# Performance work log

Measured on AMD Instinct MI355X. Metric: run time of the kernel, lower is better.

Reference implementation:

```python
import jax, jax.numpy as jnp
import numpy as np

N = 50000   # num_nodes
D = 256     # embedding_dim
R = 3       # num relations / views
E = 800000  # random edges per relation (before self-loops)
T = 8192    # target node indices
LN_EPS = 1e-5


def _build_relation(key):
    """Random graph + gcn_norm with self-loops (symmetric D^-1/2 A D^-1/2)."""
    k1, k2, k3 = jax.random.split(key, 3)
    src = jax.random.randint(k1, (E,), 0, N)
    dst = jax.random.randint(k2, (E,), 0, N)
    w = jax.random.uniform(k3, (E,))
    loop = jnp.arange(N)
    row = jnp.concatenate([src, loop])
    col = jnp.concatenate([dst, loop])
    val = jnp.concatenate([w, jnp.ones(N, jnp.float32)])
    deg = jax.ops.segment_sum(val, col, num_segments=N)
    dinv = jnp.where(deg > 0, jax.lax.rsqrt(deg), 0.0)
    val = dinv[row] * val * dinv[col]
    return row.astype(jnp.int32), col.astype(jnp.int32), val.astype(jnp.float32)


def setup_inputs() -> dict:
    key = jax.random.key(0)
    ks = jax.random.split(key, 12)
    rows, cols, vals = [], [], []
    for i in range(R):
        r, c, v = _build_relation(jax.random.fold_in(ks[0], i))
        rows.append(r); cols.append(c); vals.append(v)
    s = 1.0 / np.sqrt(D)
    inp = dict(
        node_emb=jax.random.normal(ks[1], (N, D), jnp.float32),
        W_pre=jax.random.normal(ks[2], (D, D), jnp.float32) * s,
        b_pre=jnp.zeros((D,), jnp.float32),
        g_pre=jnp.ones((D,), jnp.float32),
        be_pre=jnp.zeros((D,), jnp.float32),
        W_view=jax.random.normal(ks[3], (R, D, D), jnp.float32) * s,
        b_view=jnp.zeros((R, D), jnp.float32),
        g_view=jnp.ones((R, D), jnp.float32),
        be_view=jnp.zeros((R, D), jnp.float32),
        att_w=jax.random.normal(ks[4], (D, 1), jnp.float32) * s,
        att_b=jnp.zeros((1,), jnp.float32),
        g_fin=jnp.ones((D,), jnp.float32),
        be_fin=jnp.zeros((D,), jnp.float32),
        vals=jnp.stack(vals),            # [R, E+N]
        rows=jnp.stack(rows),            # [R, E+N] int32
        cols=jnp.stack(cols),            # [R, E+N] int32
        target_idx=jax.random.randint(ks[5], (T,), 0, N).astype(jnp.int32),
        hops=2,
    )
    return inp


def _ln(x, g, b):
    mu = jnp.mean(x, axis=-1, keepdims=True)
    var = jnp.mean(jnp.square(x - mu), axis=-1, keepdims=True)
    return (x - mu) * jax.lax.rsqrt(var + LN_EPS) * g + b


def _spmm(row, col, val, x):
    # out[i] = sum_{e: row[e]=i} val[e] * x[col[e]]
    return jax.ops.segment_sum(val[:, None] * x[col], row, num_segments=x.shape[0])


def reference(node_emb, W_pre, b_pre, g_pre, be_pre, W_view, b_view, g_view,
              be_view, att_w, att_b, g_fin, be_fin, vals, rows, cols,
              target_idx, hops):
    n = node_emb.shape[0]
    # pre_encoder: Linear + LayerNorm + GELU (exact erf gelu like torch default)
    x_graph = jax.nn.gelu(_ln(node_emb @ W_pre + b_pre, g_pre, be_pre), approximate=False)
    embeddings = []
    for i in range(rows.shape[0]):
        out = x_graph
        for _ in range(hops):
            out = _spmm(rows[i], cols[i], vals[i], out)
        out = jax.nn.gelu(_ln(out @ W_view[i] + b_view[i], g_view[i], be_view[i]),
                          approximate=False)
        embeddings.append(out)
    stack = jnp.stack(embeddings, axis=1)              # [N, R, D]
    scores = stack @ att_w + att_b                     # [N, R, 1]
    alpha = jax.nn.softmax(scores, axis=1)
    fused = jnp.sum(alpha * stack, axis=1)             # [N, D]
    control = x_graph[n - 1][None, :]
    final = jnp.concatenate([fused[: n - 1], control], axis=0)
    final = _ln(final, g_fin, be_fin)
    return final[target_idx]
```

## Files before the change

kernel.cpp:

```cpp
#include <hip/hip_runtime.h>
#include <hip/hip_bf16.h>
#include <math.h>

#define DD 256
#define BUCKET_SHIFT 9
#define BROWS 512
#define CHUNK_A 4096
#define CBLK_SHIFT 13

typedef __attribute__((ext_vector_type(8))) short short8;
typedef __attribute__((ext_vector_type(4))) float f32x4;

__device__ __forceinline__ float gelu_exact(float x) {
    return 0.5f * x * (1.0f + erff(x * 0.70710678118654752f));
}
__device__ __forceinline__ float b2f(unsigned short u) {
    unsigned int v = ((unsigned int)u) << 16;
    return __builtin_bit_cast(float, v);
}
__device__ __forceinline__ unsigned short f2b(float f) {
    __hip_bfloat16 h = __float2bfloat16(f);
    return __builtin_bit_cast(unsigned short, h);
}

__global__ __launch_bounds__(256) void part_hist(const int* __restrict__ rows,
                                                 int* __restrict__ bh,
                                                 int nnz, int NB, int nblkA) {
    int rel = blockIdx.y, blk = blockIdx.x;
    __shared__ int h[128];
    for (int b = threadIdx.x; b < NB; b += 256) h[b] = 0;
    __syncthreads();
    int base = blk * CHUNK_A;
    #pragma unroll
    for (int k = 0; k < CHUNK_A / 256; ++k) {
        int i = base + k * 256 + threadIdx.x;
        if (i < nnz) atomicAdd(&h[rows[(size_t)rel * nnz + i] >> BUCKET_SHIFT], 1);
    }
    __syncthreads();
    for (int b = threadIdx.x; b < NB; b += 256)
        bh[((size_t)(rel * NB + b)) * nblkA + blk] = h[b];
}

__global__ __launch_bounds__(256) void scan1(const int* __restrict__ cnt,
                                             int* __restrict__ rp, int* __restrict__ psum,
                                             int N, int nchunks) {
    int rel = blockIdx.x / nchunks;
    int chunk = blockIdx.x % nchunks;
    const int* c = cnt + (size_t)rel * N;
    int* out = rp + (size_t)rel * (N + 1);
    int tid = threadIdx.x, lane = tid & 63, wv = tid >> 6;
    __shared__ int wsum[4];
    int base = chunk * 1024 + tid * 4;
    int v[4];
    if (base + 3 < N) {
        int4 t4 = *(const int4*)(c + base);
        v[0] = t4.x; v[1] = t4.y; v[2] = t4.z; v[3] = t4.w;
    } else {
        #pragma unroll
        for (int q = 0; q < 4; ++q) v[q] = (base + q < N) ? c[base + q] : 0;
    }
    int tsum = v[0] + v[1] + v[2] + v[3];
    int x = tsum;
    #pragma unroll
    for (int off = 1; off < 64; off <<= 1) {
        int t = __shfl_up(x, off, 64);
        if (lane >= off) x += t;
    }
    if (lane == 63) wsum[wv] = x;
    __syncthreads();
    int woff = 0;
    #pragma unroll
    for (int k = 0; k < 4; ++k) if (k < wv) woff += wsum[k];
    int run = woff + x - tsum;
    #pragma unroll
    for (int q = 0; q < 4; ++q) {
        if (base + q < N) out[base + q] = run;
        run += v[q];
    }
    if (tid == 255) psum[rel * nchunks + chunk] = woff + x;
}

__global__ __launch_bounds__(256) void scan2(int* __restrict__ psum, int* __restrict__ rp,
                                             int N, int nchunks, int R) {
    int rel = threadIdx.x >> 6, lane = threadIdx.x & 63;
    if (rel >= R) return;
    int v = (lane < nchunks) ? psum[rel * nchunks + lane] : 0;
    int x = v;
    #pragma unroll
    for (int off = 1; off < 64; off <<= 1) {
        int t = __shfl_up(x, off, 64);
        if (lane >= off) x += t;
    }
    if (lane < nchunks) psum[rel * nchunks + lane] = x - v;
    if (lane == 63) rp[(size_t)rel * (N + 1) + N] = x;
}

__global__ __launch_bounds__(256) void scan3(int* __restrict__ rp, const int* __restrict__ psum,
                                             int N, int nchunks) {
    int rel = blockIdx.y;
    int i = blockIdx.x * 256 + threadIdx.x;
    if (i >= N) return;
    rp[(size_t)rel * (N + 1) + i] += psum[rel * nchunks + (i >> 10)];
}

__global__ __launch_bounds__(256) void part_scatter(
    const int* __restrict__ rows, const int* __restrict__ cols,
    const float* __restrict__ vals, const int* __restrict__ bhs,
    int2* __restrict__ staged, int nnz, int NB, int nblkA) {
    int rel = blockIdx.y, blk = blockIdx.x;
    __shared__ int cur[128];
    for (int b = threadIdx.x; b < NB; b += 256)
        cur[b] = bhs[((size_t)(rel * NB + b)) * nblkA + blk];
    __syncthreads();
    int base = blk * CHUNK_A;
    #pragma unroll
    for (int k = 0; k < CHUNK_A / 256; ++k) {
        int i = base + k * 256 + threadIdx.x;
        if (i < nnz) {
            int r = rows[(size_t)rel * nnz + i];
            unsigned c = (unsigned)cols[(size_t)rel * nnz + i];
            float v = vals[(size_t)rel * nnz + i];
            int pos = atomicAdd(&cur[r >> BUCKET_SHIFT], 1);
            int2 pr;
            pr.x = (int)(((unsigned)r << 16) | c);
            pr.y = __float_as_int(v);
            staged[pos] = pr;
        }
    }
}

__global__ __launch_bounds__(512) void bucket_build(
    const int2* __restrict__ staged, const int* __restrict__ bhs,
    int* __restrict__ rp, int2* __restrict__ spair,
    int nnz, int N, int NB, int nblkA, int R) {
    int rel = blockIdx.y, b = blockIdx.x;
    int start = bhs[((size_t)(rel * NB + b)) * nblkA];
    int nb1 = rel * NB + b + 1;
    int end = (nb1 < R * NB) ? bhs[(size_t)nb1 * nblkA] : R * nnz;
    int csr_base = start - rel * nnz;
    int rowbase = b << BUCKET_SHIFT;
    __shared__ int cnt2[BROWS * 8];
    __shared__ int wsum[8];
    int t = threadIdx.x, lane = t & 63, wv = t >> 6;
    #pragma unroll
    for (int q = 0; q < 8; ++q) cnt2[t + q * BROWS] = 0;
    __syncthreads();
    for (int i = start + t; i < end; i += 512) {
        unsigned p = (unsigned)staged[i].x;
        int rb = (int)(p >> 16) - rowbase;
        int cb = (int)(p & 0xFFFFu) >> CBLK_SHIFT;
        atomicAdd(&cnt2[rb * 8 + cb], 1);
    }
    __syncthreads();
    int c[8];
    int v = 0;
    #pragma unroll
    for (int q = 0; q < 8; ++q) { c[q] = cnt2[t * 8 + q]; v += c[q]; }
    int x = v;
    #pragma unroll
    for (int off = 1; off < 64; off <<= 1) {
        int tt = __shfl_up(x, off, 64);
        if (lane >= off) x += tt;
    }
    if (lane == 63) wsum[wv] = x;
    __syncthreads();
    int woff = 0;
    #pragma unroll
    for (int k = 0; k < 8; ++k) if (k < wv) woff += wsum[k];
    int excl = woff + x - v;
    __syncthreads();
    int run = excl;
    #pragma unroll
    for (int q = 0; q < 8; ++q) { cnt2[t * 8 + q] = run; run += c[q]; }
    int gr = rowbase + t;
    if (gr <= N) rp[(size_t)rel * (N + 1) + gr] = csr_base + excl;
    __syncthreads();
    for (int i = start + t; i < end; i += 512) {
        int2 s = staged[i];
        unsigned p = (unsigned)s.x;
        int rb = (int)(p >> 16) - rowbase;
        int col = (int)(p & 0xFFFFu);
        int pos = atomicAdd(&cnt2[rb * 8 + (col >> CBLK_SHIFT)], 1);
        int2 pr;
        pr.x = col;
        pr.y = s.y;
        spair[(size_t)rel * nnz + csr_base + pos] = pr;
    }
}

__global__ __launch_bounds__(256) void transpose_cast_w(
    const float* __restrict__ Wp, const float* __restrict__ Wv,
    unsigned short* __restrict__ wt) {
    __shared__ float tile[32][33];
    int m = blockIdx.y;
    int tb = blockIdx.x;
    int k0 = (tb & 7) * 32, n0 = (tb >> 3) * 32;
    const float* W = (m == 0) ? Wp : (Wv + (size_t)(m - 1) * 65536);
    int tx = threadIdx.x & 31, ty = threadIdx.x >> 5;
    #pragma unroll
    for (int i = 0; i < 4; ++i)
        tile[ty + 8 * i][tx] = W[(size_t)(k0 + ty + 8 * i) * 256 + n0 + tx];
    __syncthreads();
    #pragma unroll
    for (int i = 0; i < 4; ++i)
        wt[(size_t)m * 65536 + (size_t)(n0 + ty + 8 * i) * 256 + k0 + tx] =
            f2b(tile[tx][ty + 8 * i]);
}

template <bool A_BF16, bool OUT_BF16>
__global__ __launch_bounds__(512) void gemm_wlds(
    const void* __restrict__ Aptr, const unsigned short* __restrict__ Wt,
    const float* __restrict__ bias, const float* __restrict__ gamma,
    const float* __restrict__ beta, void* __restrict__ outp, int M, int ntiles,
    size_t aStrideB, size_t wStride, int pStride, size_t oStrideB)
{
    __shared__ __align__(16) unsigned short Wl[256 * 256];
    __shared__ float Pb[DD], Pg[DD], Pe[DD];
    const int rel = blockIdx.y;
    const char* Abase = (const char*)Aptr + (size_t)rel * aStrideB;
    char* Obase = (char*)outp + (size_t)rel * oStrideB;
    const unsigned short* Wtr = Wt + (size_t)rel * wStride;
    const int tid = threadIdx.x;
    const int lane = tid & 63;
    const int wv = tid >> 6;
    if (tid < DD) {
        Pb[tid] = bias[rel * pStride + tid];
        Pg[tid] = gamma[rel * pStride + tid];
        Pe[tid] = beta[rel * pStride + tid];
    }
    {
        int n = tid >> 1;
        int half = tid & 1;
        const unsigned short* src = Wtr + (size_t)n * DD + half * 128;
        #pragma unroll
        for (int c = 0; c < 16; ++c) {
            int c16 = half * 16 + c;
            short8 v = *(const short8*)(src + c * 8);
            *(short8*)(Wl + n * DD + ((c16 ^ (n & 7)) << 3)) = v;
        }
    }
    __syncthreads();

    const int cl = lane & 15, g = lane >> 4;

    for (int tile = blockIdx.x; tile < ntiles; tile += gridDim.x) {
        const int rbase = tile * 128 + wv * 16;
        const int arow = rbase + cl;
        const bool rok = arow < M;
        f32x4 acc[16];
        #pragma unroll
        for (int j = 0; j < 16; ++j) acc[j] = (f32x4){0.f, 0.f, 0.f, 0.f};

        #pragma unroll 2
        for (int ks = 0; ks < 8; ++ks) {
            short8 af = (short8){0,0,0,0,0,0,0,0};
            if (rok) {
                if (A_BF16) {
                    af = *(const short8*)((const unsigned short*)Abase +
                            (size_t)arow * DD + ks * 32 + g * 8);
                } else {
                    const float* ap = (const float*)Abase + (size_t)arow * DD + ks * 32 + g * 8;
                    float4 f0 = *(const float4*)ap;
                    float4 f1 = *(const float4*)(ap + 4);
                    af = (short8){(short)f2b(f0.x), (short)f2b(f0.y), (short)f2b(f0.z), (short)f2b(f0.w),
                                  (short)f2b(f1.x), (short)f2b(f1.y), (short)f2b(f1.z), (short)f2b(f1.w)};
                }
            }
            int c16 = 4 * ks + g;
            #pragma unroll
            for (int j = 0; j < 16; ++j) {
                int n = j * 16 + cl;
                short8 bf = *(const short8*)(Wl + n * DD + ((c16 ^ (n & 7)) << 3));
                acc[j] = __builtin_amdgcn_mfma_f32_16x16x32_bf16(af, bf, acc[j], 0, 0, 0);
            }
        }

        #pragma unroll
        for (int q = 0; q < 4; ++q) {
            float yv[16];
            float s = 0.f, ss = 0.f;
            #pragma unroll
            for (int j = 0; j < 16; ++j) {
                float y = acc[j][q] + Pb[cl + 16 * j];
                yv[j] = y; s += y; ss += y * y;
            }
            #pragma unroll
            for (int off = 1; off < 16; off <<= 1) {
                s  += __shfl_xor(s,  off, 16);
                ss += __shfl_xor(ss, off, 16);
            }
            float mean = s * (1.0f / DD);
            float var  = ss * (1.0f / DD) - mean * mean;
            float rstd = rsqrtf(var + 1e-5f);
            int row = rbase + g * 4 + q;
            if (row < M) {
                #pragma unroll
                for (int j = 0; j < 16; ++j) {
                    int col = cl + 16 * j;
                    float o = gelu_exact((yv[j] - mean) * rstd * Pg[col] + Pe[col]);
                    if (OUT_BF16)
                        ((unsigned short*)Obase)[(size_t)row * DD + col] = f2b(o);
                    else
                        ((float*)Obase)[(size_t)row * DD + col] = o;
                }
            }
        }
    }
}

__global__ __launch_bounds__(256) void spmm_bf(
    const int* __restrict__ rp, const int2* __restrict__ spair,
    const unsigned short* __restrict__ x, unsigned short* __restrict__ y, int N)
{
    int r = blockIdx.x * 4 + (threadIdx.x >> 6);
    if (r >= N) return;
    int lane = threadIdx.x & 63;
    int half = lane >> 5;
    int hl = lane & 31;
    int s = rp[r], e = rp[r + 1];
    float acc[8];
    #pragma unroll
    for (int k = 0; k < 8; ++k) acc[k] = 0.f;
    int j = s;
    for (; j + 4 <= e; j += 4) {
        int2 pA = spair[j + half];
        int2 pB = spair[j + 2 + half];
        short8 xa = *(const short8*)(x + (size_t)pA.x * DD + hl * 8);
        short8 xb = *(const short8*)(x + (size_t)pB.x * DD + hl * 8);
        float va = __int_as_float(pA.y), vb = __int_as_float(pB.y);
        #pragma unroll
        for (int k = 0; k < 8; ++k) {
            acc[k] += va * b2f((unsigned short)xa[k]);
            acc[k] += vb * b2f((unsigned short)xb[k]);
        }
    }
    for (; j + 2 <= e; j += 2) {
        int2 p = spair[j + half];
        short8 xv = *(const short8*)(x + (size_t)p.x * DD + hl * 8);
        float v = __int_as_float(p.y);
        #pragma unroll
        for (int k = 0; k < 8; ++k) acc[k] += v * b2f((unsigned short)xv[k]);
    }
    if (j < e && half == 0) {
        int2 p = spair[j];
        short8 xv = *(const short8*)(x + (size_t)p.x * DD + hl * 8);
        float v = __int_as_float(p.y);
        #pragma unroll
        for (int k = 0; k < 8; ++k) acc[k] += v * b2f((unsigned short)xv[k]);
    }
    #pragma unroll
    for (int k = 0; k < 8; ++k) acc[k] += __shfl_xor(acc[k], 32, 64);
    if (half == 0) {
        short8 o;
        #pragma unroll
        for (int k = 0; k < 8; ++k) o[k] = (short)f2b(acc[k]);
        *(short8*)(y + (size_t)r * DD + hl * 8) = o;
    }
}

__global__ __launch_bounds__(256) void spmm_tgt_bf(
    const int* __restrict__ rp0, const int2* __restrict__ spair0,
    const unsigned short* __restrict__ x0, const int* __restrict__ tgt,
    unsigned short* __restrict__ y0, int T, int N, int nnz)
{
    int rel = blockIdx.y;
    const int* rp = rp0 + (size_t)rel * (N + 1);
    const int2* spair = spair0 + (size_t)rel * nnz;
    const unsigned short* x = x0 + (size_t)rel * N * DD;
    unsigned short* y = y0 + (size_t)rel * T * DD;
    int sI = blockIdx.x * 4 + (threadIdx.x >> 6);
    if (sI >= T) return;
    int lane = threadIdx.x & 63;
    int half = lane >> 5;
    int hl = lane & 31;
    int r = tgt[sI];
    int s = rp[r], e = rp[r + 1];
    float acc[8];
    #pragma unroll
    for (int k = 0; k < 8; ++k) acc[k] = 0.f;
    int j = s;
    for (; j + 4 <= e; j += 4) {
        int2 pA = spair[j + half];
        int2 pB = spair[j + 2 + half];
        short8 xa = *(const short8*)(x + (size_t)pA.x * DD + hl * 8);
        short8 xb = *(const short8*)(x + (size_t)pB.x * DD + hl * 8);
        float va = __int_as_float(pA.y), vb = __int_as_float(pB.y);
        #pragma unroll
        for (int k = 0; k < 8; ++k) {
            acc[k] += va * b2f((unsigned short)xa[k]);
            acc[k] += vb * b2f((unsigned short)xb[k]);
        }
    }
    for (; j + 2 <= e; j += 2) {
        int2 p = spair[j + half];
        short8 xv = *(const short8*)(x + (size_t)p.x * DD + hl * 8);
        float v = __int_as_float(p.y);
        #pragma unroll
        for (int k = 0; k < 8; ++k) acc[k] += v * b2f((unsigned short)xv[k]);
    }
    if (j < e && half == 0) {
        int2 p = spair[j];
        short8 xv = *(const short8*)(x + (size_t)p.x * DD + hl * 8);
        float v = __int_as_float(p.y);
        #pragma unroll
        for (int k = 0; k < 8; ++k) acc[k] += v * b2f((unsigned short)xv[k]);
    }
    #pragma unroll
    for (int k = 0; k < 8; ++k) acc[k] += __shfl_xor(acc[k], 32, 64);
    if (half == 0) {
        short8 o;
        #pragma unroll
        for (int k = 0; k < 8; ++k) o[k] = (short)f2b(acc[k]);
        *(short8*)(y + (size_t)sI * DD + hl * 8) = o;
    }
}

__global__ __launch_bounds__(256) void final_kernel(
    const unsigned short* __restrict__ emb, size_t emb_stride,
    const unsigned short* __restrict__ xg,
    const float* __restrict__ att_w, const float* __restrict__ att_b,
    const float* __restrict__ g_fin, const float* __restrict__ be_fin,
    const int* __restrict__ tgt, float* __restrict__ out, int N, int T)
{
    int sI = blockIdx.x * 4 + (threadIdx.x >> 6);
    if (sI >= T) return;
    int lane = threadIdx.x & 63;
    int t = tgt[sI];
    float4 row;
    if (t == N - 1) {
        ushort4 xv = *(const ushort4*)(xg + (size_t)t * DD + lane * 4);
        row.x = b2f(xv.x); row.y = b2f(xv.y); row.z = b2f(xv.z); row.w = b2f(xv.w);
    } else {
        ushort4 u0 = *(const ushort4*)(emb + (size_t)sI * DD + lane * 4);
        ushort4 u1 = *(const ushort4*)(emb + emb_stride + (size_t)sI * DD + lane * 4);
        ushort4 u2 = *(const ushort4*)(emb + 2 * emb_stride + (size_t)sI * DD + lane * 4);
        float4 e0 = make_float4(b2f(u0.x), b2f(u0.y), b2f(u0.z), b2f(u0.w));
        float4 e1 = make_float4(b2f(u1.x), b2f(u1.y), b2f(u1.z), b2f(u1.w));
        float4 e2 = make_float4(b2f(u2.x), b2f(u2.y), b2f(u2.z), b2f(u2.w));
        float4 aw = *(const float4*)(att_w + lane * 4);
        float s0 = e0.x*aw.x + e0.y*aw.y + e0.z*aw.z + e0.w*aw.w;
        float s1 = e1.x*aw.x + e1.y*aw.y + e1.z*aw.z + e1.w*aw.w;
        float s2 = e2.x*aw.x + e2.y*aw.y + e2.z*aw.z + e2.w*aw.w;
        #pragma unroll
        for (int off = 32; off > 0; off >>= 1) {
            s0 += __shfl_xor(s0, off, 64);
            s1 += __shfl_xor(s1, off, 64);
            s2 += __shfl_xor(s2, off, 64);
        }
        float ab = att_b[0];
        s0 += ab; s1 += ab; s2 += ab;
        float m = fmaxf(s0, fmaxf(s1, s2));
        float w0 = expf(s0 - m), w1 = expf(s1 - m), w2 = expf(s2 - m);
        float inv = 1.0f / (w0 + w1 + w2);
        w0 *= inv; w1 *= inv; w2 *= inv;
        row.x = w0*e0.x + w1*e1.x + w2*e2.x;
        row.y = w0*e0.y + w1*e1.y + w2*e2.y;
        row.z = w0*e0.z + w1*e1.z + w2*e2.z;
        row.w = w0*e0.w + w1*e1.w + w2*e2.w;
    }
    float s  = row.x + row.y + row.z + row.w;
    float ss = row.x*row.x + row.y*row.y + row.z*row.z + row.w*row.w;
    #pragma unroll
    for (int off = 32; off > 0; off >>= 1) {
        s  += __shfl_xor(s,  off, 64);
        ss += __shfl_xor(ss, off, 64);
    }
    float mean = s * (1.0f / DD);
    float var  = ss * (1.0f / DD) - mean * mean;
    float rstd = rsqrtf(var + 1e-5f);
    float4 gg  = *(const float4*)(g_fin  + lane * 4);
    float4 be4 = *(const float4*)(be_fin + lane * 4);
    float4 o;
    o.x = (row.x - mean) * rstd * gg.x + be4.x;
    o.y = (row.y - mean) * rstd * gg.y + be4.y;
    o.z = (row.z - mean) * rstd * gg.z + be4.z;
    o.w = (row.w - mean) * rstd * gg.w + be4.w;
    *(float4*)(out + (size_t)sI * DD + lane * 4) = o;
}

extern "C" void kernel_launch(void* const* d_in, const int* in_sizes, int n_in,
                              void* d_out, int out_size, void* d_ws, size_t ws_size,
                              hipStream_t stream) {
    const float* node_emb = (const float*)d_in[0];
    const float* W_pre  = (const float*)d_in[1];
    const float* b_pre  = (const float*)d_in[2];
    const float* g_pre  = (const float*)d_in[3];
    const float* be_pre = (const float*)d_in[4];
    const float* W_view = (const float*)d_in[5];
    const float* b_view = (const float*)d_in[6];
    const float* g_view = (const float*)d_in[7];
    const float* be_view= (const float*)d_in[8];
    const float* att_w  = (const float*)d_in[9];
    const float* att_b  = (const float*)d_in[10];
    const float* g_fin  = (const float*)d_in[11];
    const float* be_fin = (const float*)d_in[12];
    const float* vals   = (const float*)d_in[13];
    const int*   rows   = (const int*)d_in[14];
    const int*   cols   = (const int*)d_in[15];
    const int*   tgt    = (const int*)d_in[16];

    const int N   = in_sizes[0] / DD;
    const int R   = in_sizes[5] / (DD * DD);
    const int nnz = in_sizes[13] / R;
    const int T   = in_sizes[16];

    const int NB    = (N + BROWS - 1) >> BUCKET_SHIFT;
    const int nblkA = (nnz + CHUNK_A - 1) / CHUNK_A;
    const int S     = R * NB * nblkA;
    const int nchS  = (S + 1023) / 1024;

    char* ws = (char*)d_ws;
    size_t off = 0;
    auto alloc = [&](size_t bytes) -> char* {
        char* p = ws + off;
        off += (bytes + 255) & ~(size_t)255;
        return p;
    };
    int*            rp     = (int*)alloc((size_t)R * (N + 1) * 4);
    int*            psum   = (int*)alloc(1024);
    int*            bhraw  = (int*)alloc((size_t)S * 4);
    int*            bhs    = (int*)alloc((size_t)(S + 1) * 4);
    int2*           spair  = (int2*)alloc((size_t)R * nnz * 8);
    unsigned short* xg_bf  = (unsigned short*)alloc((size_t)N * DD * 2);
    unsigned short* tmp_bf = (unsigned short*)alloc((size_t)R * N * DD * 2);
    unsigned short* ev_bf  = (unsigned short*)alloc((size_t)R * T * DD * 2);
    unsigned short* wt_bf  = (unsigned short*)alloc((size_t)(R + 1) * DD * DD * 2);
    int2* staged = (int2*)tmp_bf;
    (void)ws_size; (void)n_in; (void)out_size;

    part_hist<<<dim3(nblkA, R), 256, 0, stream>>>(rows, bhraw, nnz, NB, nblkA);
    scan1<<<nchS, 256, 0, stream>>>(bhraw, bhs, psum, S, nchS);
    scan2<<<1, 256, 0, stream>>>(psum, bhs, S, nchS, 1);
    scan3<<<dim3((S + 255) / 256, 1), 256, 0, stream>>>(bhs, psum, S, nchS);
    part_scatter<<<dim3(nblkA, R), 256, 0, stream>>>(rows, cols, vals, bhs, staged,
                                                     nnz, NB, nblkA);
    bucket_build<<<dim3(NB, R), 512, 0, stream>>>(staged, bhs, rp, spair,
                                                  nnz, N, NB, nblkA, R);

    transpose_cast_w<<<dim3(64, R + 1), 256, 0, stream>>>(W_pre, W_view, wt_bf);

    int ntiles_pre = (N + 127) / 128;
    int grid_pre = ntiles_pre < 256 ? ntiles_pre : 256;
    gemm_wlds<false, true><<<dim3(grid_pre, 1), 512, 0, stream>>>(
        node_emb, wt_bf, b_pre, g_pre, be_pre, xg_bf, N, ntiles_pre, 0, 0, 0, 0);

    for (int v = 0; v < R; ++v) {
        spmm_bf<<<(N + 3) / 4, 256, 0, stream>>>(rp + (size_t)v * (N + 1),
                                                 spair + (size_t)v * nnz, xg_bf,
                                                 tmp_bf + (size_t)v * N * DD, N);
    }

    spmm_tgt_bf<<<dim3((T + 3) / 4, R), 256, 0, stream>>>(rp, spair, tmp_bf, tgt,
                                                          ev_bf, T, N, nnz);

    int ntiles_v = (T + 127) / 128;
    gemm_wlds<true, true><<<dim3(ntiles_v, R), 512, 0, stream>>>(
        ev_bf, wt_bf + (size_t)DD * DD, b_view, g_view, be_view, ev_bf, T, ntiles_v,
        (size_t)T * DD * 2, (size_t)DD * DD, DD, (size_t)T * DD * 2);

    final_kernel<<<(T + 3) / 4, 256, 0, stream>>>(ev_bf, (size_t)T * DD, xg_bf,
                                                  att_w, att_b, g_fin, be_fin, tgt,
                                                  (float*)d_out, N, T);
}
```

Measured before the change: 340.1 us.

## Gather first-hop SpMM from FP8 copy of x_graph and shrink intermediate buffer

```diff
diff --git a/kernel.cpp b/kernel.cpp
--- a/kernel.cpp
+++ b/kernel.cpp
@@ -205,6 +205,21 @@
     for (int i = 0; i < 4; ++i)
         wt[(size_t)m * 65536 + (size_t)(n0 + ty + 8 * i) * 256 + k0 + tx] =
             f2b(tile[tx][ty + 8 * i]);
+}
+
+__global__ __launch_bounds__(256) void cast_f8(const unsigned short* __restrict__ xb,
+                                               unsigned char* __restrict__ xf, long n8) {
+    long i = (long)blockIdx.x * 256 + threadIdx.x;
+    if (i >= n8) return;
+    short8 v = *(const short8*)(xb + i * 8);
+    float f[8];
+    #pragma unroll
+    for (int k = 0; k < 8; ++k) f[k] = b2f((unsigned short)v[k]);
+    int d0 = __builtin_amdgcn_cvt_pk_fp8_f32(f[0], f[1], 0, false);
+    d0 = __builtin_amdgcn_cvt_pk_fp8_f32(f[2], f[3], d0, true);
+    int d1 = __builtin_amdgcn_cvt_pk_fp8_f32(f[4], f[5], 0, false);
+    d1 = __builtin_amdgcn_cvt_pk_fp8_f32(f[6], f[7], d1, true);
+    *(uint2*)(xf + i * 8) = make_uint2((unsigned)d0, (unsigned)d1);
 }
 
 template <bool A_BF16, bool OUT_BF16>
@@ -308,9 +323,9 @@
     }
 }
 
-__global__ __launch_bounds__(256) void spmm_bf(
+__global__ __launch_bounds__(256) void spmm_f8(
     const int* __restrict__ rp, const int2* __restrict__ spair,
-    const unsigned short* __restrict__ x, unsigned short* __restrict__ y, int N)
+    const unsigned char* __restrict__ x, unsigned short* __restrict__ y, int N)
 {
     int r = blockIdx.x * 4 + (threadIdx.x >> 6);
     if (r >= N) return;
@@ -325,28 +340,60 @@
     for (; j + 4 <= e; j += 4) {
         int2 pA = spair[j + half];
         int2 pB = spair[j + 2 + half];
-        short8 xa = *(const short8*)(x + (size_t)pA.x * DD + hl * 8);
-        short8 xb = *(const short8*)(x + (size_t)pB.x * DD + hl * 8);
+        uint2 ua = *(const uint2*)(x + (size_t)pA.x * DD + hl * 8);
+        uint2 ub = *(const uint2*)(x + (size_t)pB.x * DD + hl * 8);
         float va = __int_as_float(pA.y), vb = __int_as_float(pB.y);
-        #pragma unroll
-        for (int k = 0; k < 8; ++k) {
-            acc[k] += va * b2f((unsigned short)xa[k]);
-            acc[k] += vb * b2f((unsigned short)xb[k]);
-        }
+        float xa[8], xb[8];
+        xa[0] = __builtin_amdgcn_cvt_f32_fp8((int)ua.x, 0);
+        xa[1] = __builtin_amdgcn_cvt_f32_fp8((int)ua.x, 1);
+        xa[2] = __builtin_amdgcn_cvt_f32_fp8((int)ua.x, 2);
+        xa[3] = __builtin_amdgcn_cvt_f32_fp8((int)ua.x, 3);
+        xa[4] = __builtin_amdgcn_cvt_f32_fp8((int)ua.y, 0);
+        xa[5] = __builtin_amdgcn_cvt_f32_fp8((int)ua.y, 1);
+        xa[6] = __builtin_amdgcn_cvt_f32_fp8((int)ua.y, 2);
+        xa[7] = __builtin_amdgcn_cvt_f32_fp8((int)ua.y, 3);
+        xb[0] = __builtin_amdgcn_cvt_f32_fp8((int)ub.x, 0);
+        xb[1] = __builtin_amdgcn_cvt_f32_fp8((int)ub.x, 1);
+        xb[2] = __builtin_amdgcn_cvt_f32_fp8((int)ub.x, 2);
+        xb[3] = __builtin_amdgcn_cvt_f32_fp8((int)ub.x, 3);
+        xb[4] = __builtin_amdgcn_cvt_f32_fp8((int)ub.y, 0);
+        xb[5] = __builtin_amdgcn_cvt_f32_fp8((int)ub.y, 1);
+        xb[6] = __builtin_amdgcn_cvt_f32_fp8((int)ub.y, 2);
+        xb[7] = __builtin_amdgcn_cvt_f32_fp8((int)ub.y, 3);
+        #pragma unroll
+        for (int k = 0; k < 8; ++k) acc[k] += va * xa[k] + vb * xb[k];
     }
     for (; j + 2 <= e; j += 2) {
         int2 p = spair[j + half];
-        short8 xv = *(const short8*)(x + (size_t)p.x * DD + hl * 8);
+        uint2 ua = *(const uint2*)(x + (size_t)p.x * DD + hl * 8);
         float v = __int_as_float(p.y);
-        #pragma unroll
-        for (int k = 0; k < 8; ++k) acc[k] += v * b2f((unsigned short)xv[k]);
+        float xa[8];
+        xa[0] = __builtin_amdgcn_cvt_f32_fp8((int)ua.x, 0);
+        xa[1] = __builtin_amdgcn_cvt_f32_fp8((int)ua.x, 1);
+        xa[2] = __builtin_amdgcn_cvt_f32_fp8((int)ua.x, 2);
+        xa[3] = __builtin_amdgcn_cvt_f32_fp8((int)ua.x, 3);
+        xa[4] = __builtin_amdgcn_cvt_f32_fp8((int)ua.y, 0);
+        xa[5] = __builtin_amdgcn_cvt_f32_fp8((int)ua.y, 1);
+        xa[6] = __builtin_amdgcn_cvt_f32_fp8((int)ua.y, 2);
+        xa[7] = __builtin_amdgcn_cvt_f32_fp8((int)ua.y, 3);
+        #pragma unroll
+        for (int k = 0; k < 8; ++k) acc[k] += v * xa[k];
     }
     if (j < e && half == 0) {
         int2 p = spair[j];
-        short8 xv = *(const short8*)(x + (size_t)p.x * DD + hl * 8);
+        uint2 ua = *(const uint2*)(x + (size_t)p.x * DD + hl * 8);
         float v = __int_as_float(p.y);
-        #pragma unroll
-        for (int k = 0; k < 8; ++k) acc[k] += v * b2f((unsigned short)xv[k]);
+        float xa[8];
+        xa[0] = __builtin_amdgcn_cvt_f32_fp8((int)ua.x, 0);
+        xa[1] = __builtin_amdgcn_cvt_f32_fp8((int)ua.x, 1);
+        xa[2] = __builtin_amdgcn_cvt_f32_fp8((int)ua.x, 2);
+        xa[3] = __builtin_amdgcn_cvt_f32_fp8((int)ua.x, 3);
+        xa[4] = __builtin_amdgcn_cvt_f32_fp8((int)ua.y, 0);
+        xa[5] = __builtin_amdgcn_cvt_f32_fp8((int)ua.y, 1);
+        xa[6] = __builtin_amdgcn_cvt_f32_fp8((int)ua.y, 2);
+        xa[7] = __builtin_amdgcn_cvt_f32_fp8((int)ua.y, 3);
+        #pragma unroll
+        for (int k = 0; k < 8; ++k) acc[k] += v * xa[k];
     }
     #pragma unroll
     for (int k = 0; k < 8; ++k) acc[k] += __shfl_xor(acc[k], 32, 64);
@@ -359,15 +406,10 @@
 }
 
 __global__ __launch_bounds__(256) void spmm_tgt_bf(
-    const int* __restrict__ rp0, const int2* __restrict__ spair0,
-    const unsigned short* __restrict__ x0, const int* __restrict__ tgt,
-    unsigned short* __restrict__ y0, int T, int N, int nnz)
+    const int* __restrict__ rp, const int2* __restrict__ spair,
+    const unsigned short* __restrict__ x, const int* __restrict__ tgt,
+    unsigned short* __restrict__ y, int T)
 {
-    int rel = blockIdx.y;
-    const int* rp = rp0 + (size_t)rel * (N + 1);
-    const int2* spair = spair0 + (size_t)rel * nnz;
-    const unsigned short* x = x0 + (size_t)rel * N * DD;
-    unsigned short* y = y0 + (size_t)rel * T * DD;
     int sI = blockIdx.x * 4 + (threadIdx.x >> 6);
     if (sI >= T) return;
     int lane = threadIdx.x & 63;
@@ -522,7 +564,8 @@
     int*            bhs    = (int*)alloc((size_t)(S + 1) * 4);
     int2*           spair  = (int2*)alloc((size_t)R * nnz * 8);
     unsigned short* xg_bf  = (unsigned short*)alloc((size_t)N * DD * 2);
-    unsigned short* tmp_bf = (unsigned short*)alloc((size_t)R * N * DD * 2);
+    unsigned char*  xg_f8  = (unsigned char*)alloc((size_t)N * DD);
+    unsigned short* tmp_bf = (unsigned short*)alloc((size_t)N * DD * 2);
     unsigned short* ev_bf  = (unsigned short*)alloc((size_t)R * T * DD * 2);
     unsigned short* wt_bf  = (unsigned short*)alloc((size_t)(R + 1) * DD * DD * 2);
     int2* staged = (int2*)tmp_bf;
@@ -544,14 +587,16 @@
     gemm_wlds<false, true><<<dim3(grid_pre, 1), 512, 0, stream>>>(
         node_emb, wt_bf, b_pre, g_pre, be_pre, xg_bf, N, ntiles_pre, 0, 0, 0, 0);
 
+    long n8 = (long)N * DD / 8;
+    cast_f8<<<(int)((n8 + 255) / 256), 256, 0, stream>>>(xg_bf, xg_f8, n8);
+
     for (int v = 0; v < R; ++v) {
-        spmm_bf<<<(N + 3) / 4, 256, 0, stream>>>(rp + (size_t)v * (N + 1),
-                                                 spair + (size_t)v * nnz, xg_bf,
-                                                 tmp_bf + (size_t)v * N * DD, N);
-    }
-
-    spmm_tgt_bf<<<dim3((T + 3) / 4, R), 256, 0, stream>>>(rp, spair, tmp_bf, tgt,
-                                                          ev_bf, T, N, nnz);
+        const int* rpv = rp + (size_t)v * (N + 1);
+        const int2* spv = spair + (size_t)v * nnz;
+        spmm_f8<<<(N + 3) / 4, 256, 0, stream>>>(rpv, spv, xg_f8, tmp_bf, N);
+        spmm_tgt_bf<<<(T + 3) / 4, 256, 0, stream>>>(rpv, spv, tmp_bf, tgt,
+                                                     ev_bf + (size_t)v * T * DD, T);
+    }
 
     int ntiles_v = (T + 127) / 128;
     gemm_wlds<true, true><<<dim3(ntiles_v, R), 512, 0, stream>>>(
```

After: 300.2 us. 1.13x faster.
